# Optimization experiments

Measured on AMD Instinct MI355X. Metric: run time of the kernel, lower is better.

Reference implementation:

```python
import jax, jax.numpy as jnp
import numpy as np

NEG = -1e10

def setup_inputs() -> dict:
    key = jax.random.key(0)
    ks = jax.random.split(key, 12)
    B, W, V, D, R, VOCAB = 16, 64, 64, 256, 64, 50000
    head_ctx = jax.random.randint(ks[0], (B, W), 0, VOCAB)
    tail_ctx = jax.random.randint(ks[1], (B, V), 0, VOCAB)
    emb = jax.random.normal(ks[2], (VOCAB, D), dtype=jnp.float32) * 0.02
    rela_mat = jax.random.normal(ks[3], (R, D), dtype=jnp.float32) * 0.02
    fc_w = jax.random.normal(ks[4], (3 * D, D), dtype=jnp.float32) * (1.0 / np.sqrt(3 * D))
    fc_b = jnp.zeros((D,), jnp.float32)
    att_w1 = jax.random.normal(ks[5], (D, D), dtype=jnp.float32) * (1.0 / np.sqrt(D))
    att_b1 = jnp.zeros((D,), jnp.float32)
    att_w2 = jax.random.normal(ks[6], (D, 1), dtype=jnp.float32) * (1.0 / np.sqrt(D))
    att_b2 = jnp.zeros((1,), jnp.float32)
    out_w = jax.random.normal(ks[7], (D, 1), dtype=jnp.float32) * (1.0 / np.sqrt(D))
    out_b = jnp.zeros((1,), jnp.float32)
    return {"head_ctx": head_ctx, "tail_ctx": tail_ctx, "emb": emb, "rela_mat": rela_mat,
            "fc_w": fc_w, "fc_b": fc_b, "att_w1": att_w1, "att_b1": att_b1,
            "att_w2": att_w2, "att_b2": att_b2, "out_w": out_w, "out_b": out_b}

def reference(head_ctx, tail_ctx, emb, rela_mat, fc_w, fc_b, att_w1, att_b1, att_w2, att_b2, out_w, out_b):
    A = emb[head_ctx]            # [B, W, D]
    Bt = emb[tail_ctx]           # [B, V, D]
    Bsz, W, D = A.shape
    V = Bt.shape[1]
    R = rela_mat.shape[0]
    N = W * V
    # DistMult scoring for every (head_i, tail_j, rela_r) triple, no repeat materialization
    scores = jnp.einsum('bid,bjd,rd->bijr', A, Bt, rela_mat).reshape(Bsz, N, R)
    # cut_rela_score: mask relations not beating the null (last) relation
    null = scores[:, :, -1:]
    scores = jnp.where(scores <= null, NEG, scores)
    norm_scores = jax.nn.softmax(scores, axis=-1)            # [B, N, R]
    rela_vec = jnp.einsum('bnr,rd->bnd', norm_scores, rela_mat)
    # tuple (i,j) pairing: index n = i*V + j
    A_rep = jnp.broadcast_to(A[:, :, None, :], (Bsz, W, V, D)).reshape(Bsz, N, D)
    B_rep = jnp.broadcast_to(Bt[:, None, :, :], (Bsz, W, V, D)).reshape(Bsz, N, D)
    tuple_vec = jnp.tanh(jnp.concatenate([A_rep, B_rep, rela_vec], axis=-1) @ fc_w + fc_b)  # [B, N, D]
    # tuple attention pooling
    att = jnp.tanh(tuple_vec @ att_w1 + att_b1) @ att_w2 + att_b2   # [B, N, 1]
    att_norms = jax.nn.softmax(att, axis=1)                          # [B, N, 1]
    fuse = jnp.sum(att_norms * tuple_vec, axis=1)                    # [B, D]
    logits = (fuse @ out_w + out_b).squeeze(-1)                      # [B]
    return logits, att_norms, norm_scores
```

## Files before the change

kernel.cpp:

```cpp
#include <hip/hip_runtime.h>
#include <hip/hip_bf16.h>

#define NB 16
#define NW 64
#define NV 64
#define ND 256
#define NR 64
#define NN 4096
#define NEGV -10000000000.0f

typedef __attribute__((ext_vector_type(8))) short short8;
typedef __attribute__((ext_vector_type(4))) float f32x4;

__device__ inline float cvt(const void* p, int idx, int flag) {
  if (flag) return __bfloat162float(((const __hip_bfloat16*)p)[idx]);
  return ((const float*)p)[idx];
}
__device__ inline void stv(void* p, int idx, float v, int flag) {
  if (flag) ((__hip_bfloat16*)p)[idx] = __float2bfloat16(v);
  else ((float*)p)[idx] = v;
}
__device__ inline float bf2f(short s) {
  return __uint_as_float(((unsigned int)(unsigned short)s) << 16);
}
__device__ inline float tanh_fast(float x) {
  float ax = fabsf(x);
  float e = __expf(-2.f * ax);
  float r = (1.f - e) / (1.f + e);
  return copysignf(r, x);
}

__global__ void k_detect(const unsigned int* embw, int* flagp) {
  __shared__ float red[256];
  int t = threadIdx.x;
  float mx = 0.f;
  for (int i = t; i < 1024; i += 256) {
    unsigned int w = embw[i];
    unsigned int fb = (w & 0xffffu) << 16;
    float a = fabsf(__uint_as_float(fb));
    if (!(a < 1e9f)) a = 1e9f;
    mx = fmaxf(mx, a);
  }
  red[t] = mx;
  __syncthreads();
  for (int s = 128; s > 0; s >>= 1) {
    if (t < s) red[t] = fmaxf(red[t], red[t + s]);
    __syncthreads();
  }
  if (t == 0) flagp[0] = (red[0] < 1000.f) ? 1 : 0;
}

__global__ void k_prep(const void* rela, float* relaT,
                       const void* b1, const void* w2, const void* outw,
                       const void* b2, const void* outb, float* sp,
                       const void* w1, __hip_bfloat16* w1b,
                       const int* head, const int* tail, const void* emb,
                       float* Af, float* Bf, const int* flagp) {
  int flag = flagp[0];
  int blk = blockIdx.x;
  int t = threadIdx.x;
  if (blk < 64) {
    relaT[t * NR + blk] = cvt(rela, blk * ND + t, flag);
  } else if (blk == 64) {
    sp[t] = cvt(b1, t, flag);
    sp[256 + t] = cvt(w2, t, flag);
    sp[512 + t] = cvt(outw, t, flag);
    if (t == 0) {
      sp[768] = cvt(b2, 0, flag);
      sp[769] = cvt(outb, 0, flag);
    }
  } else if (blk < 321) {
    int flat = (blk - 65) * 256 + t;
    int i = flat & 7;
    int lane = (flat >> 3) & 63;
    int kst = (flat >> 9) & 7;
    int nt = flat >> 12;
    int k = kst * 32 + (lane >> 4) * 8 + i;
    int n = nt * 16 + (lane & 15);
    w1b[flat] = __float2bfloat16(cvt(w1, k * ND + n, flag));
  } else {
    int row = blk - 321;
    if (row < NB * NW) {
      int ix = head[row];
      Af[row * ND + t] = cvt(emb, ix * ND + t, flag);
    } else {
      int rr = row - NB * NW;
      int ix = tail[rr];
      Bf[rr * ND + t] = cvt(emb, ix * ND + t, flag);
    }
  }
}

__global__ void __launch_bounds__(256) k_premm(const float* Af, const float* Bf,
                                               const void* rela, const void* fcw,
                                               const void* fcb, float* Ah,
                                               float* Bh, __hip_bfloat16* rwb,
                                               const int* flagp) {
  int flag = flagp[0];
  int blk = blockIdx.x;
  int t = threadIdx.x;
  __shared__ float rl[4][ND];
  int base, wbase, addb = 0, isr = 0;
  const float* src = Af;
  if (blk < 256) { base = blk * 4; wbase = 0; addb = 1; }
  else if (blk < 512) { base = (blk - 256) * 4; src = Bf; wbase = ND; }
  else { base = (blk - 512) * 4; wbase = 2 * ND; isr = 1; }
#pragma unroll
  for (int i = 0; i < 4; ++i)
    rl[i][t] = isr ? cvt(rela, (base + i) * ND + t, flag)
                   : src[(base + i) * ND + t];
  __syncthreads();
  float acc0 = 0.f, acc1 = 0.f, acc2 = 0.f, acc3 = 0.f;
  const f32x4* r0p = (const f32x4*)rl[0];
  const f32x4* r1p = (const f32x4*)rl[1];
  const f32x4* r2p = (const f32x4*)rl[2];
  const f32x4* r3p = (const f32x4*)rl[3];
  for (int k4 = 0; k4 < 64; ++k4) {
    float w0 = cvt(fcw, (wbase + k4 * 4 + 0) * ND + t, flag);
    float w1v = cvt(fcw, (wbase + k4 * 4 + 1) * ND + t, flag);
    float w2v = cvt(fcw, (wbase + k4 * 4 + 2) * ND + t, flag);
    float w3v = cvt(fcw, (wbase + k4 * 4 + 3) * ND + t, flag);
    f32x4 r0 = r0p[k4], r1 = r1p[k4], r2 = r2p[k4], r3 = r3p[k4];
    acc0 += r0.x * w0 + r0.y * w1v + r0.z * w2v + r0.w * w3v;
    acc1 += r1.x * w0 + r1.y * w1v + r1.z * w2v + r1.w * w3v;
    acc2 += r2.x * w0 + r2.y * w1v + r2.z * w2v + r2.w * w3v;
    acc3 += r3.x * w0 + r3.y * w1v + r3.z * w2v + r3.w * w3v;
  }
  float bias = addb ? cvt(fcb, t, flag) : 0.f;
  float res[4] = {acc0 + bias, acc1 + bias, acc2 + bias, acc3 + bias};
  if (!isr) {
    float* dst = addb ? Ah : Bh;
#pragma unroll
    for (int i = 0; i < 4; ++i) dst[(base + i) * ND + t] = res[i];
  } else {
#pragma unroll
    for (int i = 0; i < 4; ++i) {
      int rr = base + i;
      int ks = rr >> 5, ii = rr & 7, lh = (rr >> 3) & 3;
      int nt = t >> 4, ll = t & 15;
      int flat = ((nt * 2 + ks) * 64 + lh * 16 + ll) * 8 + ii;
      rwb[flat] = __float2bfloat16(res[i]);
    }
  }
}

__global__ void __launch_bounds__(256) k_scores(const float* Af, const float* Bf,
                                                const float* relaT, void* out,
                                                __hip_bfloat16* nsb,
                                                const int* flagp) {
  int flag = flagp[0];
  int bi = blockIdx.x;
  int b = bi >> 6;
  int t = threadIdx.x;
  int r = t & 63;
  int q = t >> 6;
  __shared__ float Al[ND];
  __shared__ float Bl[4 * ND];
  __shared__ float part[4 * 256];
  Al[t] = Af[bi * ND + t];
  __syncthreads();
  float preR[64];
#pragma unroll
  for (int i2 = 0; i2 < 64; ++i2) {
    int d = q * 64 + i2;
    preR[i2] = Al[d] * relaT[d * NR + r];
  }
  const f32x4* Bl4 = (const f32x4*)Bl;
  for (int jg = 0; jg < 16; ++jg) {
#pragma unroll
    for (int jj = 0; jj < 4; ++jj)
      Bl[jj * ND + t] = Bf[(b * NV + jg * 4 + jj) * ND + t];
    __syncthreads();
#pragma unroll
    for (int jj = 0; jj < 4; ++jj) {
      float acc = 0.f;
      int ib = jj * 64 + q * 16;
#pragma unroll
      for (int i4 = 0; i4 < 16; ++i4) {
        f32x4 bv = Bl4[ib + i4];
        acc += preR[i4 * 4 + 0] * bv.x;
        acc += preR[i4 * 4 + 1] * bv.y;
        acc += preR[i4 * 4 + 2] * bv.z;
        acc += preR[i4 * 4 + 3] * bv.w;
      }
      part[jj * 256 + t] = acc;
    }
    __syncthreads();
    {
      int j4 = q;
      float s = part[j4 * 256 + r] + part[j4 * 256 + 64 + r]
              + part[j4 * 256 + 128 + r] + part[j4 * 256 + 192 + r];
      float nullv = __shfl(s, 63, 64);
      float m = (s <= nullv) ? NEGV : s;
      float mx = m;
#pragma unroll
      for (int o = 32; o > 0; o >>= 1) mx = fmaxf(mx, __shfl_xor(mx, o, 64));
      float e = __expf(m - mx);
      float sum = e;
#pragma unroll
      for (int o = 32; o > 0; o >>= 1) sum += __shfl_xor(sum, o, 64);
      float ns = e / sum;
      int j = jg * 4 + j4;
      int nidx = (bi * 64 + j) * 64 + r;
      stv(out, 16 + NB * NN + nidx, ns, flag);
      nsb[nidx] = __float2bfloat16(ns);
    }
    __syncthreads();
  }
}

__global__ void __launch_bounds__(256) k_tuple2(const __hip_bfloat16* nsb,
                                                const __hip_bfloat16* rwb,
                                                const float* Ah, const float* Bh,
                                                __hip_bfloat16* tup) {
  int t = threadIdx.x;
  int wv = t >> 6, lane = t & 63;
  int bi = blockIdx.x;
  int b = bi >> 6;
  const short* nsS = (const short*)nsb;
  const short* rwS = (const short*)rwb;
  int m = lane & 15;
  int kgrp = lane >> 4;
  f32x4 acc[16];
#pragma unroll
  for (int i = 0; i < 16; ++i) acc[i] = (f32x4){0.f, 0.f, 0.f, 0.f};
  int nrow = bi * 64 + wv * 16 + m;
#pragma unroll
  for (int ks = 0; ks < 2; ++ks) {
    short8 a = *(const short8*)(nsS + (size_t)nrow * 64 + ks * 32 + kgrp * 8);
#pragma unroll
    for (int nt = 0; nt < 16; ++nt) {
      short8 bfr = *(const short8*)(rwS + (((nt * 2 + ks) * 64 + lane) << 3));
      acc[nt] = __builtin_amdgcn_mfma_f32_16x16x32_bf16(a, bfr, acc[nt], 0, 0, 0);
    }
  }
  int rbase = bi * 64 + wv * 16 + (lane >> 4) * 4;
  int jbase = rbase & 63;
#pragma unroll
  for (int nt = 0; nt < 16; ++nt) {
    int col = nt * 16 + m;
    float ahv = Ah[bi * ND + col];
#pragma unroll
    for (int reg = 0; reg < 4; ++reg) {
      int ng = rbase + reg;
      float v = acc[nt][reg] + ahv + Bh[(size_t)(b * 64 + jbase + reg) * ND + col];
      tup[(size_t)ng * ND + col] = __float2bfloat16(tanh_fast(v));
    }
  }
}

__global__ void __launch_bounds__(256) k_att2(const __hip_bfloat16* tup,
                                              const __hip_bfloat16* w1b,
                                              const float* sp,
                                              float* att_raw, float* dotv) {
  int t = threadIdx.x;
  int wv = t >> 6, lane = t & 63;
  int r0 = blockIdx.x * 128 + wv * 32;
  const short* tupS = (const short*)tup;
  const short* w1S = (const short*)w1b;
  const float* owf = sp + 512;
  float b2v = sp[768];

  f32x4 acc0[16], acc1[16];
#pragma unroll
  for (int i = 0; i < 16; ++i) {
    acc0[i] = (f32x4){0.f, 0.f, 0.f, 0.f};
    acc1[i] = (f32x4){0.f, 0.f, 0.f, 0.f};
  }
  float dp0 = 0.f, dp1 = 0.f;
  int arow0 = r0 + (lane & 15);
  int arow1 = arow0 + 16;
  int kgrp = lane >> 4;

#pragma unroll
  for (int ks = 0; ks < 8; ++ks) {
    int k0 = ks * 32 + kgrp * 8;
    short8 a0 = *(const short8*)(tupS + (size_t)arow0 * ND + k0);
    short8 a1 = *(const short8*)(tupS + (size_t)arow1 * ND + k0);
#pragma unroll
    for (int i = 0; i < 8; ++i) {
      float w = owf[k0 + i];
      dp0 += bf2f(a0[i]) * w;
      dp1 += bf2f(a1[i]) * w;
    }
#pragma unroll
    for (int nt = 0; nt < 16; ++nt) {
      short8 bfr = *(const short8*)(w1S + (((nt * 8 + ks) * 64 + lane) << 3));
      acc0[nt] = __builtin_amdgcn_mfma_f32_16x16x32_bf16(a0, bfr, acc0[nt], 0, 0, 0);
      acc1[nt] = __builtin_amdgcn_mfma_f32_16x16x32_bf16(a1, bfr, acc1[nt], 0, 0, 0);
    }
  }

  dp0 += __shfl_xor(dp0, 16, 64); dp0 += __shfl_xor(dp0, 32, 64);
  dp1 += __shfl_xor(dp1, 16, 64); dp1 += __shfl_xor(dp1, 32, 64);
  if (lane < 16) {
    dotv[r0 + lane] = dp0;
    dotv[r0 + 16 + lane] = dp1;
  }

  float p0[4] = {0.f, 0.f, 0.f, 0.f};
  float p1[4] = {0.f, 0.f, 0.f, 0.f};
#pragma unroll
  for (int nt = 0; nt < 16; ++nt) {
    int col = nt * 16 + (lane & 15);
    float b1v = sp[col];
    float w2v = sp[256 + col];
#pragma unroll
    for (int reg = 0; reg < 4; ++reg) {
      p0[reg] += tanh_fast(acc0[nt][reg] + b1v) * w2v;
      p1[reg] += tanh_fast(acc1[nt][reg] + b1v) * w2v;
    }
  }
#pragma unroll
  for (int o = 1; o < 16; o <<= 1) {
#pragma unroll
    for (int reg = 0; reg < 4; ++reg) {
      p0[reg] += __shfl_xor(p0[reg], o, 64);
      p1[reg] += __shfl_xor(p1[reg], o, 64);
    }
  }
  if ((lane & 15) == 0) {
    int rb = r0 + (lane >> 4) * 4;
#pragma unroll
    for (int reg = 0; reg < 4; ++reg) {
      att_raw[rb + reg] = p0[reg] + b2v;
      att_raw[rb + 16 + reg] = p1[reg] + b2v;
    }
  }
}

__global__ void k_fuse(const float* att_raw, const float* dotv,
                       const float* sp, void* out, const int* flagp) {
  int flag = flagp[0];
  int b = blockIdx.x;
  int t = threadIdx.x;
  __shared__ float red[256];
  float vals[16];
  float mx = -3.4e38f;
#pragma unroll
  for (int c = 0; c < 16; ++c) {
    vals[c] = att_raw[b * NN + c * 256 + t];
    mx = fmaxf(mx, vals[c]);
  }
  red[t] = mx;
  __syncthreads();
  for (int s = 128; s > 0; s >>= 1) {
    if (t < s) red[t] = fmaxf(red[t], red[t + s]);
    __syncthreads();
  }
  float M = red[0];
  __syncthreads();
  float sm = 0.f;
#pragma unroll
  for (int c = 0; c < 16; ++c) {
    vals[c] = __expf(vals[c] - M);
    sm += vals[c];
  }
  red[t] = sm;
  __syncthreads();
  for (int s = 128; s > 0; s >>= 1) {
    if (t < s) red[t] += red[t + s];
    __syncthreads();
  }
  float Z = red[0];
  __syncthreads();
  float acc = 0.f;
#pragma unroll
  for (int c = 0; c < 16; ++c) {
    int n = c * 256 + t;
    float a = vals[c] / Z;
    stv(out, 16 + b * NN + n, a, flag);
    acc += a * dotv[b * NN + n];
  }
  red[t] = acc;
  __syncthreads();
  for (int s = 128; s > 0; s >>= 1) {
    if (t < s) red[t] += red[t + s];
    __syncthreads();
  }
  if (t == 0) stv(out, b, red[0] + sp[769], flag);
}

extern "C" void kernel_launch(void* const* d_in, const int* in_sizes, int n_in,
                              void* d_out, int out_size, void* d_ws, size_t ws_size,
                              hipStream_t stream) {
  const int* head = (const int*)d_in[0];
  const int* tail = (const int*)d_in[1];
  const void* emb = d_in[2];
  const void* rela = d_in[3];
  const void* fcw = d_in[4];
  const void* fcb = d_in[5];
  const void* w1 = d_in[6];
  const void* b1 = d_in[7];
  const void* w2 = d_in[8];
  const void* b2 = d_in[9];
  const void* outw = d_in[10];
  const void* outb = d_in[11];

  float* ws = (float*)d_ws;
  int* flagp = (int*)d_ws;
  const size_t O_RELAT = 16;
  const size_t O_AF = O_RELAT + 16384;
  const size_t O_BF = O_AF + 262144;
  const size_t O_AH = O_BF + 262144;
  const size_t O_BH = O_AH + 262144;
  const size_t O_ATTR = O_BH + 262144;
  const size_t O_DOT = O_ATTR + 65536;
  const size_t O_SP = O_DOT + 65536;
  const size_t O_W1B = O_SP + 1024;
  const size_t O_RWB = O_W1B + 32768;
  const size_t O_NSB = O_RWB + 8192;
  const size_t O_TUP = O_NSB + 2097152;

  float* relaT = ws + O_RELAT;
  float* Af = ws + O_AF;
  float* Bf = ws + O_BF;
  float* Ah = ws + O_AH;
  float* Bh = ws + O_BH;
  float* attr = ws + O_ATTR;
  float* dotv = ws + O_DOT;
  float* sp = ws + O_SP;
  __hip_bfloat16* w1b = (__hip_bfloat16*)(ws + O_W1B);
  __hip_bfloat16* rwb = (__hip_bfloat16*)(ws + O_RWB);
  __hip_bfloat16* nsb = (__hip_bfloat16*)(ws + O_NSB);
  __hip_bfloat16* tup = (__hip_bfloat16*)(ws + O_TUP);

  hipLaunchKernelGGL(k_detect, dim3(1), dim3(256), 0, stream,
                     (const unsigned int*)emb, flagp);
  hipLaunchKernelGGL(k_prep, dim3(2369), dim3(256), 0, stream,
                     rela, relaT, b1, w2, outw, b2, outb, sp,
                     w1, w1b, head, tail, emb, Af, Bf, flagp);
  hipLaunchKernelGGL(k_premm, dim3(528), dim3(256), 0, stream,
                     Af, Bf, rela, fcw, fcb, Ah, Bh, rwb, flagp);
  hipLaunchKernelGGL(k_scores, dim3(1024), dim3(256), 0, stream,
                     Af, Bf, relaT, d_out, nsb, flagp);
  hipLaunchKernelGGL(k_tuple2, dim3(1024), dim3(256), 0, stream,
                     nsb, rwb, Ah, Bh, tup);
  hipLaunchKernelGGL(k_att2, dim3(512), dim3(256), 0, stream,
                     tup, w1b, sp, attr, dotv);
  hipLaunchKernelGGL(k_fuse, dim3(16), dim3(256), 0, stream,
                     attr, dotv, sp, d_out, flagp);
}
```

Baseline: 265.2 us.

## Fuse tuple and attention kernels via LDS tile, drop Bl staging in scores

Merges the tuple-vector kernel and the attention MLP kernel into one, keeping each block's 64x256 bf16 tanh tile in padded shared memory instead of writing and rereading a 4M-element global buffer. The scores kernel now reads B rows straight from global memory (with a wave-uniform q) rather than staging them in LDS, and k_premm gets restrict qualifiers and partial unrolling. This saves the tuple round-trip and one launch, at the cost of 33KB of LDS per block, which lowers occupancy. The fused kernel also runs one 16-row MFMA chain per wave instead of two.

Measured after the change: 299.4 us. +12.9%, slower.

```diff
diff --git a/kernel.cpp b/kernel.cpp
--- a/kernel.cpp
+++ b/kernel.cpp
@@ -91,11 +91,15 @@
   }
 }
 
-__global__ void __launch_bounds__(256) k_premm(const float* Af, const float* Bf,
-                                               const void* rela, const void* fcw,
-                                               const void* fcb, float* Ah,
-                                               float* Bh, __hip_bfloat16* rwb,
-                                               const int* flagp) {
+__global__ void __launch_bounds__(256) k_premm(const float* __restrict__ Af,
+                                               const float* __restrict__ Bf,
+                                               const void* __restrict__ rela,
+                                               const void* __restrict__ fcw,
+                                               const void* __restrict__ fcb,
+                                               float* __restrict__ Ah,
+                                               float* __restrict__ Bh,
+                                               __hip_bfloat16* __restrict__ rwb,
+                                               const int* __restrict__ flagp) {
   int flag = flagp[0];
   int blk = blockIdx.x;
   int t = threadIdx.x;
@@ -115,6 +119,7 @@
   const f32x4* r1p = (const f32x4*)rl[1];
   const f32x4* r2p = (const f32x4*)rl[2];
   const f32x4* r3p = (const f32x4*)rl[3];
+#pragma unroll 4
   for (int k4 = 0; k4 < 64; ++k4) {
     float w0 = cvt(fcw, (wbase + k4 * 4 + 0) * ND + t, flag);
     float w1v = cvt(fcw, (wbase + k4 * 4 + 1) * ND + t, flag);
@@ -144,18 +149,19 @@
   }
 }
 
-__global__ void __launch_bounds__(256) k_scores(const float* Af, const float* Bf,
-                                                const float* relaT, void* out,
-                                                __hip_bfloat16* nsb,
-                                                const int* flagp) {
+__global__ void __launch_bounds__(256) k_scores(const float* __restrict__ Af,
+                                                const float* __restrict__ Bf,
+                                                const float* __restrict__ relaT,
+                                                void* __restrict__ out,
+                                                __hip_bfloat16* __restrict__ nsb,
+                                                const int* __restrict__ flagp) {
   int flag = flagp[0];
   int bi = blockIdx.x;
   int b = bi >> 6;
   int t = threadIdx.x;
   int r = t & 63;
-  int q = t >> 6;
+  int q = __builtin_amdgcn_readfirstlane(t >> 6);
   __shared__ float Al[ND];
-  __shared__ float Bl[4 * ND];
   __shared__ float part[4 * 256];
   Al[t] = Af[bi * ND + t];
   __syncthreads();
@@ -165,23 +171,18 @@
     int d = q * 64 + i2;
     preR[i2] = Al[d] * relaT[d * NR + r];
   }
-  const f32x4* Bl4 = (const f32x4*)Bl;
+  const float* __restrict__ Bbase = Bf + (size_t)b * NV * ND + q * 64;
   for (int jg = 0; jg < 16; ++jg) {
 #pragma unroll
-    for (int jj = 0; jj < 4; ++jj)
-      Bl[jj * ND + t] = Bf[(b * NV + jg * 4 + jj) * ND + t];
-    __syncthreads();
-#pragma unroll
     for (int jj = 0; jj < 4; ++jj) {
+      const float* __restrict__ Bj = Bbase + (size_t)(jg * 4 + jj) * ND;
       float acc = 0.f;
-      int ib = jj * 64 + q * 16;
 #pragma unroll
       for (int i4 = 0; i4 < 16; ++i4) {
-        f32x4 bv = Bl4[ib + i4];
-        acc += preR[i4 * 4 + 0] * bv.x;
-        acc += preR[i4 * 4 + 1] * bv.y;
-        acc += preR[i4 * 4 + 2] * bv.z;
-        acc += preR[i4 * 4 + 3] * bv.w;
+        acc += preR[i4 * 4 + 0] * Bj[i4 * 4 + 0];
+        acc += preR[i4 * 4 + 1] * Bj[i4 * 4 + 1];
+        acc += preR[i4 * 4 + 2] * Bj[i4 * 4 + 2];
+        acc += preR[i4 * 4 + 3] * Bj[i4 * 4 + 3];
       }
       part[jj * 256 + t] = acc;
     }
@@ -209,18 +210,22 @@
   }
 }
 
-__global__ void __launch_bounds__(256) k_tuple2(const __hip_bfloat16* nsb,
-                                                const __hip_bfloat16* rwb,
-                                                const float* Ah, const float* Bh,
-                                                __hip_bfloat16* tup) {
+__global__ void __launch_bounds__(256) k_tupatt(
+    const __hip_bfloat16* __restrict__ nsb, const __hip_bfloat16* __restrict__ rwb,
+    const float* __restrict__ Ah, const float* __restrict__ Bh,
+    const __hip_bfloat16* __restrict__ w1b, const float* __restrict__ sp,
+    float* __restrict__ att_raw, float* __restrict__ dotv) {
+  __shared__ __align__(16) short tl[64 * 264];
   int t = threadIdx.x;
   int wv = t >> 6, lane = t & 63;
   int bi = blockIdx.x;
   int b = bi >> 6;
   const short* nsS = (const short*)nsb;
   const short* rwS = (const short*)rwb;
+  const short* w1S = (const short*)w1b;
   int m = lane & 15;
   int kgrp = lane >> 4;
+
   f32x4 acc[16];
 #pragma unroll
   for (int i = 0; i < 16; ++i) acc[i] = (f32x4){0.f, 0.f, 0.f, 0.f};
@@ -234,98 +239,64 @@
       acc[nt] = __builtin_amdgcn_mfma_f32_16x16x32_bf16(a, bfr, acc[nt], 0, 0, 0);
     }
   }
-  int rbase = bi * 64 + wv * 16 + (lane >> 4) * 4;
-  int jbase = rbase & 63;
+  int rl0 = wv * 16 + kgrp * 4;
 #pragma unroll
   for (int nt = 0; nt < 16; ++nt) {
     int col = nt * 16 + m;
     float ahv = Ah[bi * ND + col];
 #pragma unroll
     for (int reg = 0; reg < 4; ++reg) {
-      int ng = rbase + reg;
-      float v = acc[nt][reg] + ahv + Bh[(size_t)(b * 64 + jbase + reg) * ND + col];
-      tup[(size_t)ng * ND + col] = __float2bfloat16(tanh_fast(v));
-    }
-  }
-}
-
-__global__ void __launch_bounds__(256) k_att2(const __hip_bfloat16* tup,
-                                              const __hip_bfloat16* w1b,
-                                              const float* sp,
-                                              float* att_raw, float* dotv) {
-  int t = threadIdx.x;
-  int wv = t >> 6, lane = t & 63;
-  int r0 = blockIdx.x * 128 + wv * 32;
-  const short* tupS = (const short*)tup;
-  const short* w1S = (const short*)w1b;
+      float v = acc[nt][reg] + ahv + Bh[(size_t)(b * 64 + rl0 + reg) * ND + col];
+      __hip_bfloat16 hb = __float2bfloat16(tanh_fast(v));
+      tl[(rl0 + reg) * 264 + col] = *(short*)&hb;
+    }
+  }
+  __syncthreads();
+
   const float* owf = sp + 512;
   float b2v = sp[768];
-
-  f32x4 acc0[16], acc1[16];
-#pragma unroll
-  for (int i = 0; i < 16; ++i) {
-    acc0[i] = (f32x4){0.f, 0.f, 0.f, 0.f};
-    acc1[i] = (f32x4){0.f, 0.f, 0.f, 0.f};
-  }
-  float dp0 = 0.f, dp1 = 0.f;
-  int arow0 = r0 + (lane & 15);
-  int arow1 = arow0 + 16;
-  int kgrp = lane >> 4;
-
+  f32x4 acc2[16];
+#pragma unroll
+  for (int i = 0; i < 16; ++i) acc2[i] = (f32x4){0.f, 0.f, 0.f, 0.f};
+  float dp = 0.f;
+  int arow = wv * 16 + m;
 #pragma unroll
   for (int ks = 0; ks < 8; ++ks) {
     int k0 = ks * 32 + kgrp * 8;
-    short8 a0 = *(const short8*)(tupS + (size_t)arow0 * ND + k0);
-    short8 a1 = *(const short8*)(tupS + (size_t)arow1 * ND + k0);
-#pragma unroll
-    for (int i = 0; i < 8; ++i) {
-      float w = owf[k0 + i];
-      dp0 += bf2f(a0[i]) * w;
-      dp1 += bf2f(a1[i]) * w;
-    }
+    short8 a = *(const short8*)(tl + arow * 264 + k0);
+#pragma unroll
+    for (int i = 0; i < 8; ++i) dp += bf2f(a[i]) * owf[k0 + i];
 #pragma unroll
     for (int nt = 0; nt < 16; ++nt) {
       short8 bfr = *(const short8*)(w1S + (((nt * 8 + ks) * 64 + lane) << 3));
-      acc0[nt] = __builtin_amdgcn_mfma_f32_16x16x32_bf16(a0, bfr, acc0[nt], 0, 0, 0);
-      acc1[nt] = __builtin_amdgcn_mfma_f32_16x16x32_bf16(a1, bfr, acc1[nt], 0, 0, 0);
-    }
-  }
-
-  dp0 += __shfl_xor(dp0, 16, 64); dp0 += __shfl_xor(dp0, 32, 64);
-  dp1 += __shfl_xor(dp1, 16, 64); dp1 += __shfl_xor(dp1, 32, 64);
-  if (lane < 16) {
-    dotv[r0 + lane] = dp0;
-    dotv[r0 + 16 + lane] = dp1;
-  }
+      acc2[nt] = __builtin_amdgcn_mfma_f32_16x16x32_bf16(a, bfr, acc2[nt], 0, 0, 0);
+    }
+  }
+  dp += __shfl_xor(dp, 16, 64);
+  dp += __shfl_xor(dp, 32, 64);
+  if (lane < 16) dotv[bi * 64 + wv * 16 + lane] = dp;
 
   float p0[4] = {0.f, 0.f, 0.f, 0.f};
-  float p1[4] = {0.f, 0.f, 0.f, 0.f};
 #pragma unroll
   for (int nt = 0; nt < 16; ++nt) {
-    int col = nt * 16 + (lane & 15);
+    int col = nt * 16 + m;
     float b1v = sp[col];
     float w2v = sp[256 + col];
 #pragma unroll
-    for (int reg = 0; reg < 4; ++reg) {
-      p0[reg] += tanh_fast(acc0[nt][reg] + b1v) * w2v;
-      p1[reg] += tanh_fast(acc1[nt][reg] + b1v) * w2v;
-    }
+    for (int reg = 0; reg < 4; ++reg)
+      p0[reg] += tanh_fast(acc2[nt][reg] + b1v) * w2v;
   }
 #pragma unroll
   for (int o = 1; o < 16; o <<= 1) {
 #pragma unroll
-    for (int reg = 0; reg < 4; ++reg) {
+    for (int reg = 0; reg < 4; ++reg)
       p0[reg] += __shfl_xor(p0[reg], o, 64);
-      p1[reg] += __shfl_xor(p1[reg], o, 64);
-    }
-  }
-  if ((lane & 15) == 0) {
-    int rb = r0 + (lane >> 4) * 4;
-#pragma unroll
-    for (int reg = 0; reg < 4; ++reg) {
+  }
+  if (m == 0) {
+    int rb = bi * 64 + wv * 16 + kgrp * 4;
+#pragma unroll
+    for (int reg = 0; reg < 4; ++reg)
       att_raw[rb + reg] = p0[reg] + b2v;
-      att_raw[rb + 16 + reg] = p1[reg] + b2v;
-    }
   }
 }
 
@@ -410,7 +381,6 @@
   const size_t O_W1B = O_SP + 1024;
   const size_t O_RWB = O_W1B + 32768;
   const size_t O_NSB = O_RWB + 8192;
-  const size_t O_TUP = O_NSB + 2097152;
 
   float* relaT = ws + O_RELAT;
   float* Af = ws + O_AF;
@@ -423,7 +393,6 @@
   __hip_bfloat16* w1b = (__hip_bfloat16*)(ws + O_W1B);
   __hip_bfloat16* rwb = (__hip_bfloat16*)(ws + O_RWB);
   __hip_bfloat16* nsb = (__hip_bfloat16*)(ws + O_NSB);
-  __hip_bfloat16* tup = (__hip_bfloat16*)(ws + O_TUP);
 
   hipLaunchKernelGGL(k_detect, dim3(1), dim3(256), 0, stream,
                      (const unsigned int*)emb, flagp);
@@ -434,10 +403,8 @@
                      Af, Bf, rela, fcw, fcb, Ah, Bh, rwb, flagp);
   hipLaunchKernelGGL(k_scores, dim3(1024), dim3(256), 0, stream,
                      Af, Bf, relaT, d_out, nsb, flagp);
-  hipLaunchKernelGGL(k_tuple2, dim3(1024), dim3(256), 0, stream,
-                     nsb, rwb, Ah, Bh, tup);
-  hipLaunchKernelGGL(k_att2, dim3(512), dim3(256), 0, stream,
-                     tup, w1b, sp, attr, dotv);
+  hipLaunchKernelGGL(k_tupatt, dim3(1024), dim3(256), 0, stream,
+                     nsb, rwb, Ah, Bh, w1b, sp, attr, dotv);
   hipLaunchKernelGGL(k_fuse, dim3(16), dim3(256), 0, stream,
                      attr, dotv, sp, d_out, flagp);
 }
```

## Read B rows directly from global in k_scores with double-buffered partials

Applied to the files above, without the earlier changes.

k_scores no longer stages tail embeddings through shared memory. Each wave reads its 64-element slice of B directly from global memory, with a wave-uniform q so the loads can become scalar loads. The partial-sum buffer is double-buffered so one of the two __syncthreads per iteration can be dropped. __restrict__ qualifiers and an unroll pragma are also added across several kernels to help the compiler schedule loads, at the cost of relying on the cache for B reuse.

Result: no change. 262.5 us (-1.0%).

```diff
diff --git a/kernel.cpp b/kernel.cpp
--- a/kernel.cpp
+++ b/kernel.cpp
@@ -91,11 +91,15 @@
   }
 }
 
-__global__ void __launch_bounds__(256) k_premm(const float* Af, const float* Bf,
-                                               const void* rela, const void* fcw,
-                                               const void* fcb, float* Ah,
-                                               float* Bh, __hip_bfloat16* rwb,
-                                               const int* flagp) {
+__global__ void __launch_bounds__(256) k_premm(const float* __restrict__ Af,
+                                               const float* __restrict__ Bf,
+                                               const void* __restrict__ rela,
+                                               const void* __restrict__ fcw,
+                                               const void* __restrict__ fcb,
+                                               float* __restrict__ Ah,
+                                               float* __restrict__ Bh,
+                                               __hip_bfloat16* __restrict__ rwb,
+                                               const int* __restrict__ flagp) {
   int flag = flagp[0];
   int blk = blockIdx.x;
   int t = threadIdx.x;
@@ -115,6 +119,7 @@
   const f32x4* r1p = (const f32x4*)rl[1];
   const f32x4* r2p = (const f32x4*)rl[2];
   const f32x4* r3p = (const f32x4*)rl[3];
+#pragma unroll 4
   for (int k4 = 0; k4 < 64; ++k4) {
     float w0 = cvt(fcw, (wbase + k4 * 4 + 0) * ND + t, flag);
     float w1v = cvt(fcw, (wbase + k4 * 4 + 1) * ND + t, flag);
@@ -144,19 +149,20 @@
   }
 }
 
-__global__ void __launch_bounds__(256) k_scores(const float* Af, const float* Bf,
-                                                const float* relaT, void* out,
-                                                __hip_bfloat16* nsb,
-                                                const int* flagp) {
+__global__ void __launch_bounds__(256) k_scores(const float* __restrict__ Af,
+                                                const float* __restrict__ Bf,
+                                                const float* __restrict__ relaT,
+                                                void* __restrict__ out,
+                                                __hip_bfloat16* __restrict__ nsb,
+                                                const int* __restrict__ flagp) {
   int flag = flagp[0];
   int bi = blockIdx.x;
   int b = bi >> 6;
   int t = threadIdx.x;
   int r = t & 63;
-  int q = t >> 6;
+  int q = __builtin_amdgcn_readfirstlane(t >> 6);
   __shared__ float Al[ND];
-  __shared__ float Bl[4 * ND];
-  __shared__ float part[4 * 256];
+  __shared__ float part[2][4 * 256];
   Al[t] = Af[bi * ND + t];
   __syncthreads();
   float preR[64];
@@ -165,31 +171,27 @@
     int d = q * 64 + i2;
     preR[i2] = Al[d] * relaT[d * NR + r];
   }
-  const f32x4* Bl4 = (const f32x4*)Bl;
+  const float* __restrict__ Bbase = Bf + (size_t)b * NV * ND + q * 64;
   for (int jg = 0; jg < 16; ++jg) {
-#pragma unroll
-    for (int jj = 0; jj < 4; ++jj)
-      Bl[jj * ND + t] = Bf[(b * NV + jg * 4 + jj) * ND + t];
-    __syncthreads();
+    float* pb = part[jg & 1];
 #pragma unroll
     for (int jj = 0; jj < 4; ++jj) {
+      const float* __restrict__ Bj = Bbase + (size_t)(jg * 4 + jj) * ND;
       float acc = 0.f;
-      int ib = jj * 64 + q * 16;
 #pragma unroll
       for (int i4 = 0; i4 < 16; ++i4) {
-        f32x4 bv = Bl4[ib + i4];
-        acc += preR[i4 * 4 + 0] * bv.x;
-        acc += preR[i4 * 4 + 1] * bv.y;
-        acc += preR[i4 * 4 + 2] * bv.z;
-        acc += preR[i4 * 4 + 3] * bv.w;
+        acc += preR[i4 * 4 + 0] * Bj[i4 * 4 + 0];
+        acc += preR[i4 * 4 + 1] * Bj[i4 * 4 + 1];
+        acc += preR[i4 * 4 + 2] * Bj[i4 * 4 + 2];
+        acc += preR[i4 * 4 + 3] * Bj[i4 * 4 + 3];
       }
-      part[jj * 256 + t] = acc;
+      pb[jj * 256 + t] = acc;
     }
     __syncthreads();
     {
       int j4 = q;
-      float s = part[j4 * 256 + r] + part[j4 * 256 + 64 + r]
-              + part[j4 * 256 + 128 + r] + part[j4 * 256 + 192 + r];
+      float s = pb[j4 * 256 + r] + pb[j4 * 256 + 64 + r]
+              + pb[j4 * 256 + 128 + r] + pb[j4 * 256 + 192 + r];
       float nullv = __shfl(s, 63, 64);
       float m = (s <= nullv) ? NEGV : s;
       float mx = m;
@@ -205,14 +207,14 @@
       stv(out, 16 + NB * NN + nidx, ns, flag);
       nsb[nidx] = __float2bfloat16(ns);
     }
-    __syncthreads();
-  }
-}
-
-__global__ void __launch_bounds__(256) k_tuple2(const __hip_bfloat16* nsb,
-                                                const __hip_bfloat16* rwb,
-                                                const float* Ah, const float* Bh,
-                                                __hip_bfloat16* tup) {
+  }
+}
+
+__global__ void __launch_bounds__(256) k_tuple2(const __hip_bfloat16* __restrict__ nsb,
+                                                const __hip_bfloat16* __restrict__ rwb,
+                                                const float* __restrict__ Ah,
+                                                const float* __restrict__ Bh,
+                                                __hip_bfloat16* __restrict__ tup) {
   int t = threadIdx.x;
   int wv = t >> 6, lane = t & 63;
   int bi = blockIdx.x;
@@ -249,10 +251,11 @@
   }
 }
 
-__global__ void __launch_bounds__(256) k_att2(const __hip_bfloat16* tup,
-                                              const __hip_bfloat16* w1b,
-                                              const float* sp,
-                                              float* att_raw, float* dotv) {
+__global__ void __launch_bounds__(256) k_att2(const __hip_bfloat16* __restrict__ tup,
+                                              const __hip_bfloat16* __restrict__ w1b,
+                                              const float* __restrict__ sp,
+                                              float* __restrict__ att_raw,
+                                              float* __restrict__ dotv) {
   int t = threadIdx.x;
   int wv = t >> 6, lane = t & 63;
   int r0 = blockIdx.x * 128 + wv * 32;
```
